# Kernel tuning notes

Measured on AMD Instinct MI355X. Metric: run time of the kernel, lower is better.

The kernel has to match this reference:

```python
import jax, jax.numpy as jnp
import numpy as np

D_MODEL, N_HEADS, N_KV, HEAD_DIM, D_LAT = 1024, 8, 2, 128, 32
N_REP = N_HEADS // N_KV  # 4
B, T = 2, 2048


def setup_inputs() -> dict:
    key = jax.random.key(0)
    ks = jax.random.split(key, 8)
    s = lambda fan_in: 1.0 / np.sqrt(fan_in)
    return {
        "x": jax.random.normal(ks[0], (B, T, D_MODEL), jnp.float32),
        # weights stored as [in, out] (transpose of torch Linear.weight)
        "wq": jax.random.normal(ks[1], (D_MODEL, N_HEADS * HEAD_DIM), jnp.float32) * s(D_MODEL),
        "wk_down": jax.random.normal(ks[2], (D_MODEL, N_KV * D_LAT), jnp.float32) * s(D_MODEL),
        "wv_down": jax.random.normal(ks[3], (D_MODEL, N_KV * D_LAT), jnp.float32) * s(D_MODEL),
        "wk_up": jax.random.normal(ks[4], (D_LAT, HEAD_DIM), jnp.float32) * s(D_LAT),
        "wv_up": jax.random.normal(ks[5], (D_LAT, HEAD_DIM), jnp.float32) * s(D_LAT),
        "wo": jax.random.normal(ks[6], (N_HEADS * HEAD_DIM, D_MODEL), jnp.float32) * s(N_HEADS * HEAD_DIM),
    }


def reference(x, wq, wk_down, wv_down, wk_up, wv_up, wo):
    Bq, Tq, _ = x.shape
    scale = HEAD_DIM ** -0.5  # SDPA default scale
    # Q: [B,T,Hkv,Rep,Dh] (grouped view avoids materializing repeated K/V)
    q = (x @ wq).reshape(Bq, Tq, N_KV, N_REP, HEAD_DIM)
    # latent KV: [B,T,Hkv,Dl] -> up-project to [B,T,Hkv,Dh]
    k_lat = (x @ wk_down).reshape(Bq, Tq, N_KV, D_LAT)
    v_lat = (x @ wv_down).reshape(Bq, Tq, N_KV, D_LAT)
    k = jnp.einsum("bkhl,ld->bkhd", k_lat, wk_up)
    v = jnp.einsum("bkhl,ld->bkhd", v_lat, wv_up)
    # causal attention, GQA via grouped einsum (no repeat_interleave copy)
    scores = jnp.einsum("bqhrd,bkhd->bhrqk", q, k) * scale  # [B,Hkv,Rep,T,T]
    causal = jnp.tril(jnp.ones((Tq, Tq), dtype=bool))
    scores = jnp.where(causal, scores, jnp.finfo(scores.dtype).min)
    probs = jax.nn.softmax(scores, axis=-1)
    y = jnp.einsum("bhrqk,bkhd->bqhrd", probs, v)  # [B,T,Hkv,Rep,Dh]
    y = y.reshape(Bq, Tq, N_HEADS * HEAD_DIM)
    return y @ wo
```

## Files before the change

### kernel.cpp

```cpp
#include <hip/hip_runtime.h>
#include <hip/hip_bf16.h>


typedef __bf16 bf16_t;
typedef bf16_t bf16x8 __attribute__((ext_vector_type(8)));
typedef float f32x4 __attribute__((ext_vector_type(4)));

__device__ inline bf16x8 cvt8(const float* __restrict__ p) {
  f32x4 a = *(const f32x4*)p, b = *(const f32x4*)(p + 4);
  bf16x8 r;
#pragma unroll
  for (int i = 0; i < 4; ++i) { r[i] = (bf16_t)a[i]; r[4 + i] = (bf16_t)b[i]; }
  return r;
}

__global__ __launch_bounds__(256) void prep_mfma(
    const float* __restrict__ x, const float* __restrict__ wq,
    const float* __restrict__ wkd, const float* __restrict__ wvd,
    const float* __restrict__ wku, const float* __restrict__ wvu,
    const float* __restrict__ wo, bf16_t* __restrict__ Xb,
    bf16_t* __restrict__ WqkvT, bf16_t* __restrict__ WcombT) {
  __shared__ __align__(16) char smem[34816];
  const int tid = threadIdx.x;
  const int wave = tid >> 6, lane = tid & 63;
  const int quad = lane >> 4, col = lane & 15;
  const int bi = blockIdx.x;

  if (bi < 64) {
    const int h = bi >> 3;
    const int c0 = (bi & 7) * 128 + wave * 32;
    f32x4 acc[2][2];
#pragma unroll
    for (int i = 0; i < 2; ++i)
#pragma unroll
      for (int j = 0; j < 2; ++j) acc[i][j] = (f32x4){0.f, 0.f, 0.f, 0.f};
#pragma unroll
    for (int ks = 0; ks < 4; ++ks) {
      const int ko = ks * 32 + quad * 8;
      bf16x8 a0 = cvt8(wku + col * 128 + ko);
      bf16x8 a1 = cvt8(wku + (16 + col) * 128 + ko);
      bf16x8 b0 = cvt8(wq + (size_t)(c0 + col) * 1024 + h * 128 + ko);
      bf16x8 b1 = cvt8(wq + (size_t)(c0 + 16 + col) * 1024 + h * 128 + ko);
      acc[0][0] = __builtin_amdgcn_mfma_f32_16x16x32_bf16(a0, b0, acc[0][0], 0, 0, 0);
      acc[0][1] = __builtin_amdgcn_mfma_f32_16x16x32_bf16(a0, b1, acc[0][1], 0, 0, 0);
      acc[1][0] = __builtin_amdgcn_mfma_f32_16x16x32_bf16(a1, b0, acc[1][0], 0, 0, 0);
      acc[1][1] = __builtin_amdgcn_mfma_f32_16x16x32_bf16(a1, b1, acc[1][1], 0, 0, 0);
    }
#pragma unroll
    for (int ms = 0; ms < 2; ++ms)
#pragma unroll
      for (int ns = 0; ns < 2; ++ns)
#pragma unroll
        for (int v = 0; v < 4; ++v)
          WqkvT[(size_t)(h * 32 + ms * 16 + quad * 4 + v) * 1024 + c0 + ns * 16 + col] =
              (bf16_t)acc[ms][ns][v];
  } else if (bi < 128) {
    const int b2 = bi - 64;
    const int h = b2 >> 3, m0 = (b2 & 7) * 128;
    bf16_t(*B_lds)[136] = (bf16_t(*)[136])smem;
    {
      const int d = tid >> 1, mh = (tid & 1) * 64;
      const float* wp = wo + (size_t)(h * 128 + d) * 1024 + m0 + mh;
#pragma unroll
      for (int i = 0; i < 16; ++i) {
        f32x4 w4 = *(const f32x4*)(wp + i * 4);
#pragma unroll
        for (int t = 0; t < 4; ++t) B_lds[mh + i * 4 + t][d] = (bf16_t)w4[t];
      }
    }
    __syncthreads();
    f32x4 acc[2][2];
#pragma unroll
    for (int i = 0; i < 2; ++i)
#pragma unroll
      for (int j = 0; j < 2; ++j) acc[i][j] = (f32x4){0.f, 0.f, 0.f, 0.f};
#pragma unroll
    for (int ks = 0; ks < 4; ++ks) {
      const int ko = ks * 32 + quad * 8;
      bf16x8 a0 = cvt8(wvu + col * 128 + ko);
      bf16x8 a1 = cvt8(wvu + (16 + col) * 128 + ko);
      bf16x8 b0 = *(const bf16x8*)&B_lds[wave * 32 + col][ko];
      bf16x8 b1 = *(const bf16x8*)&B_lds[wave * 32 + 16 + col][ko];
      acc[0][0] = __builtin_amdgcn_mfma_f32_16x16x32_bf16(a0, b0, acc[0][0], 0, 0, 0);
      acc[0][1] = __builtin_amdgcn_mfma_f32_16x16x32_bf16(a0, b1, acc[0][1], 0, 0, 0);
      acc[1][0] = __builtin_amdgcn_mfma_f32_16x16x32_bf16(a1, b0, acc[1][0], 0, 0, 0);
      acc[1][1] = __builtin_amdgcn_mfma_f32_16x16x32_bf16(a1, b1, acc[1][1], 0, 0, 0);
    }
#pragma unroll
    for (int ms = 0; ms < 2; ++ms)
#pragma unroll
      for (int ns = 0; ns < 2; ++ns)
#pragma unroll
        for (int v = 0; v < 4; ++v)
          WcombT[(size_t)(m0 + wave * 32 + ns * 16 + col) * 256 +
                 h * 32 + ms * 16 + quad * 4 + v] = (bf16_t)acc[ms][ns][v];
  } else if (bi < 160) {
    const int b3 = bi - 128;
    const int mat = b3 >> 4, c0 = (b3 & 15) * 64;
    const float* in = mat ? wvd : wkd;
    bf16_t(*tT)[72] = (bf16_t(*)[72])smem;
    {
      const int cc = tid >> 2, jq = (tid & 3) * 16;
      const float* ip = in + (size_t)(c0 + cc) * 64 + jq;
#pragma unroll
      for (int q = 0; q < 4; ++q) {
        f32x4 v4 = *(const f32x4*)(ip + q * 4);
#pragma unroll
        for (int t = 0; t < 4; ++t) tT[jq + q * 4 + t][cc] = (bf16_t)v4[t];
      }
    }
    __syncthreads();
    {
      const int j = tid >> 2, cq = (tid & 3) * 16;
      bf16_t* op = WqkvT + (size_t)(256 + mat * 64 + j) * 1024 + c0 + cq;
      *(bf16x8*)op = *(const bf16x8*)&tT[j][cq];
      *(bf16x8*)(op + 8) = *(const bf16x8*)&tT[j][cq + 8];
    }
  } else {
    const size_t base = (size_t)(bi - 160) * 32768;
    const float* ip = x + base;
    bf16_t* op = Xb + base;
#pragma unroll
    for (int it = 0; it < 16; ++it) {
      const int o = it * 2048 + tid * 8;
      *(bf16x8*)(op + o) = cvt8(ip + o);
    }
  }
}

__global__ __launch_bounds__(256) void gemm_qkv(
    const bf16_t* __restrict__ A, const bf16_t* __restrict__ Bt,
    bf16_t* __restrict__ C) {
  __shared__ bf16_t As[32][72];
  __shared__ bf16_t Bs[128][72];
  const int tid = threadIdx.x;
  const int wave = tid >> 6, lane = tid & 63;
  const int quad = lane >> 4, col = lane & 15;
  const int wm = (wave >> 1) * 16, wn = (wave & 1) * 64;
  const int m0 = blockIdx.y * 32, n0 = blockIdx.x * 128;

  f32x4 acc[4];
#pragma unroll
  for (int j = 0; j < 4; ++j) acc[j] = (f32x4){0.f, 0.f, 0.f, 0.f};

  const int ar = tid >> 3, ac = (tid & 7) * 8;
  const int br = tid >> 1, bc = (tid & 1) * 32;
  const bf16_t* aP = A + (size_t)(m0 + ar) * 1024 + ac;
  const bf16_t* bP = Bt + (size_t)(n0 + br) * 1024 + bc;

  bf16x8 aR0 = *(const bf16x8*)aP;
  bf16x8 bR0 = *(const bf16x8*)bP, bR1 = *(const bf16x8*)(bP + 8);
  bf16x8 bR2 = *(const bf16x8*)(bP + 16), bR3 = *(const bf16x8*)(bP + 24);

  for (int kt = 0; kt < 16; ++kt) {
    *(bf16x8*)&As[ar][ac] = aR0;
    *(bf16x8*)&Bs[br][bc] = bR0; *(bf16x8*)&Bs[br][bc + 8] = bR1;
    *(bf16x8*)&Bs[br][bc + 16] = bR2; *(bf16x8*)&Bs[br][bc + 24] = bR3;
    __syncthreads();
    if (kt < 15) {
      const int k0 = (kt + 1) * 64;
      aR0 = *(const bf16x8*)(aP + k0);
      bR0 = *(const bf16x8*)(bP + k0); bR1 = *(const bf16x8*)(bP + k0 + 8);
      bR2 = *(const bf16x8*)(bP + k0 + 16); bR3 = *(const bf16x8*)(bP + k0 + 24);
    }
#pragma unroll
    for (int ks = 0; ks < 2; ++ks) {
      bf16x8 af = *(const bf16x8*)&As[wm + col][ks * 32 + quad * 8];
      bf16x8 bfr[4];
#pragma unroll
      for (int j = 0; j < 4; ++j) bfr[j] = *(const bf16x8*)&Bs[wn + j * 16 + col][ks * 32 + quad * 8];
#pragma unroll
      for (int j = 0; j < 4; ++j)
        acc[j] = __builtin_amdgcn_mfma_f32_16x16x32_bf16(af, bfr[j], acc[j], 0, 0, 0);
    }
    __syncthreads();
  }

#pragma unroll
  for (int j = 0; j < 4; ++j) {
    const int cg = n0 + wn + j * 16 + col;
#pragma unroll
    for (int v = 0; v < 4; ++v)
      C[(size_t)(m0 + wm + quad * 4 + v) * 384 + cg] = (bf16_t)acc[j][v];
  }
}

__global__ __launch_bounds__(256) void gemm_out(
    const bf16_t* __restrict__ A, const bf16_t* __restrict__ Bt,
    float* __restrict__ C) {
  __shared__ bf16_t As[64][72];
  __shared__ bf16_t Bs[128][72];
  const int tid = threadIdx.x;
  const int wave = tid >> 6, lane = tid & 63;
  const int quad = lane >> 4, col = lane & 15;
  const int wm = (wave >> 1) * 32, wn = (wave & 1) * 64;
  const int m0 = blockIdx.y * 64, n0 = blockIdx.x * 128;

  f32x4 acc[2][4];
#pragma unroll
  for (int i = 0; i < 2; ++i)
#pragma unroll
    for (int j = 0; j < 4; ++j) acc[i][j] = (f32x4){0.f, 0.f, 0.f, 0.f};

  const int ar = tid >> 2, ac = (tid & 3) * 16;
  const int br = tid >> 1, bc = (tid & 1) * 32;
  const bf16_t* aP = A + (size_t)(m0 + ar) * 384 + ac;
  const bf16_t* bP = Bt + (size_t)(n0 + br) * 256 + bc;

  bf16x8 aR0 = *(const bf16x8*)aP, aR1 = *(const bf16x8*)(aP + 8);
  bf16x8 bR0 = *(const bf16x8*)bP, bR1 = *(const bf16x8*)(bP + 8);
  bf16x8 bR2 = *(const bf16x8*)(bP + 16), bR3 = *(const bf16x8*)(bP + 24);

  for (int kt = 0; kt < 4; ++kt) {
    *(bf16x8*)&As[ar][ac] = aR0; *(bf16x8*)&As[ar][ac + 8] = aR1;
    *(bf16x8*)&Bs[br][bc] = bR0; *(bf16x8*)&Bs[br][bc + 8] = bR1;
    *(bf16x8*)&Bs[br][bc + 16] = bR2; *(bf16x8*)&Bs[br][bc + 24] = bR3;
    __syncthreads();
    if (kt < 3) {
      const int k0 = (kt + 1) * 64;
      aR0 = *(const bf16x8*)(aP + k0); aR1 = *(const bf16x8*)(aP + k0 + 8);
      bR0 = *(const bf16x8*)(bP + k0); bR1 = *(const bf16x8*)(bP + k0 + 8);
      bR2 = *(const bf16x8*)(bP + k0 + 16); bR3 = *(const bf16x8*)(bP + k0 + 24);
    }
#pragma unroll
    for (int ks = 0; ks < 2; ++ks) {
      bf16x8 af[2], bfr[4];
#pragma unroll
      for (int i = 0; i < 2; ++i) af[i] = *(const bf16x8*)&As[wm + i * 16 + col][ks * 32 + quad * 8];
#pragma unroll
      for (int j = 0; j < 4; ++j) bfr[j] = *(const bf16x8*)&Bs[wn + j * 16 + col][ks * 32 + quad * 8];
#pragma unroll
      for (int i = 0; i < 2; ++i)
#pragma unroll
        for (int j = 0; j < 4; ++j)
          acc[i][j] = __builtin_amdgcn_mfma_f32_16x16x32_bf16(af[i], bfr[j], acc[i][j], 0, 0, 0);
    }
    __syncthreads();
  }

#pragma unroll
  for (int i = 0; i < 2; ++i) {
    const int rg = m0 + wm + i * 16 + quad * 4;
#pragma unroll
    for (int j = 0; j < 4; ++j) {
      const int cg = n0 + wn + j * 16 + col;
#pragma unroll
      for (int v = 0; v < 4; ++v)
        C[(size_t)(rg + v) * 1024 + cg] = acc[i][j][v];
    }
  }
}

__global__ __launch_bounds__(256, 3) void attn_lat(bf16_t* QKV) {
  const int bi = blockIdx.x;
  const int half = bi >> 8, rest = bi & 255;
  const int qt = half ? 127 - (rest >> 1) : (rest >> 1);
  const int hkv = rest & 1, b = half;
  const int tid = threadIdx.x;
  const int wave = tid >> 6, lane = tid & 63;
  const int quad = lane >> 4, col = lane & 15;

  __shared__ bf16_t Ks[2][128][36];
  __shared__ bf16_t Vt[2][32][132];
  __shared__ bf16_t Ps[4][16][132];

  const int qb = qt * 16;
  const size_t rowbase = (size_t)b * 2048;
  const int qcol0 = (hkv * 4 + wave) * 32;

  bf16x8 a_q = *(const bf16x8*)(QKV + (rowbase + qb + col) * 384 + qcol0 + quad * 8);

  f32x4 o0 = (f32x4){0.f, 0.f, 0.f, 0.f};
  f32x4 o1 = (f32x4){0.f, 0.f, 0.f, 0.f};
  float lsum[4] = {0.f, 0.f, 0.f, 0.f};

  const int nkt = (qb >> 7) + 1;
  const float scale = 0.08838834764831843f;

  const int kr = tid >> 1, dc = (tid & 1) * 16;
  const bf16_t* kvBase = QKV + (rowbase + kr) * 384 + 256 + hkv * 32 + dc;

  {
    bf16x8 kA = *(const bf16x8*)kvBase, kB = *(const bf16x8*)(kvBase + 8);
    bf16x8 vA = *(const bf16x8*)(kvBase + 64), vB = *(const bf16x8*)(kvBase + 72);
    *(bf16x8*)&Ks[0][kr][dc] = kA;
    *(bf16x8*)&Ks[0][kr][dc + 8] = kB;
#pragma unroll
    for (int t = 0; t < 8; ++t) { Vt[0][dc + t][kr] = vA[t]; Vt[0][dc + 8 + t][kr] = vB[t]; }
  }
  __syncthreads();

  for (int kt = 0; kt < nkt; ++kt) {
    const int cur = kt & 1;
    const int kb = kt * 128;
    const bool more = (kt + 1 < nkt);

    bf16x8 kA, kB, vA, vB;
    if (more) {
      const bf16_t* np = kvBase + (size_t)(kt + 1) * 128 * 384;
      kA = *(const bf16x8*)np; kB = *(const bf16x8*)(np + 8);
      vA = *(const bf16x8*)(np + 64); vB = *(const bf16x8*)(np + 72);
    }

    f32x4 s[8];
#pragma unroll
    for (int k8 = 0; k8 < 8; ++k8) {
      bf16x8 bk = *(const bf16x8*)&Ks[cur][k8 * 16 + col][quad * 8];
      s[k8] = __builtin_amdgcn_mfma_f32_16x16x32_bf16(a_q, bk, (f32x4){0.f, 0.f, 0.f, 0.f}, 0, 0, 0);
    }

    const bool full = (kb + 128 <= qb);
#pragma unroll
    for (int v = 0; v < 4; ++v) {
      const int qr = quad * 4 + v;
      const int qg = qb + qr;
#pragma unroll
      for (int k8 = 0; k8 < 8; ++k8) {
        float xx = s[k8][v] * scale;
        if (!full && (kb + k8 * 16 + col > qg)) xx = -1e30f;
        const float p = __expf(xx);
        lsum[v] += p;
        Ps[wave][qr][k8 * 16 + col] = (bf16_t)p;
      }
    }
    __asm__ __volatile__("" ::: "memory");

#pragma unroll
    for (int kc = 0; kc < 4; ++kc) {
      bf16x8 a_p = *(const bf16x8*)&Ps[wave][col][kc * 32 + quad * 8];
      bf16x8 bv0 = *(const bf16x8*)&Vt[cur][col][kc * 32 + quad * 8];
      bf16x8 bv1 = *(const bf16x8*)&Vt[cur][16 + col][kc * 32 + quad * 8];
      o0 = __builtin_amdgcn_mfma_f32_16x16x32_bf16(a_p, bv0, o0, 0, 0, 0);
      o1 = __builtin_amdgcn_mfma_f32_16x16x32_bf16(a_p, bv1, o1, 0, 0, 0);
    }

    if (more) {
      *(bf16x8*)&Ks[cur ^ 1][kr][dc] = kA;
      *(bf16x8*)&Ks[cur ^ 1][kr][dc + 8] = kB;
#pragma unroll
      for (int t = 0; t < 8; ++t) { Vt[cur ^ 1][dc + t][kr] = vA[t]; Vt[cur ^ 1][dc + 8 + t][kr] = vB[t]; }
    }
    __syncthreads();
  }

#pragma unroll
  for (int v = 0; v < 4; ++v) {
    float l = lsum[v];
#pragma unroll
    for (int off = 8; off; off >>= 1) l += __shfl_xor(l, off, 64);
    const float inv = 1.f / l;
    const size_t r = (rowbase + qb + quad * 4 + v) * 384 + qcol0;
    QKV[r + col] = (bf16_t)(o0[v] * inv);
    QKV[r + 16 + col] = (bf16_t)(o1[v] * inv);
  }
}

extern "C" void kernel_launch(void* const* d_in, const int* in_sizes, int n_in,
                              void* d_out, int out_size, void* d_ws, size_t ws_size,
                              hipStream_t stream) {
  (void)in_sizes; (void)n_in; (void)out_size; (void)ws_size;
  const float* x   = (const float*)d_in[0];
  const float* wq  = (const float*)d_in[1];
  const float* wkd = (const float*)d_in[2];
  const float* wvd = (const float*)d_in[3];
  const float* wku = (const float*)d_in[4];
  const float* wvu = (const float*)d_in[5];
  const float* wo  = (const float*)d_in[6];
  float* out = (float*)d_out;

  bf16_t* WqkvT  = (bf16_t*)d_ws;
  bf16_t* WcombT = WqkvT + (size_t)384 * 1024;
  bf16_t* QKV    = WcombT + (size_t)1024 * 256;
  bf16_t* Xb     = QKV + (size_t)4096 * 384;

  prep_mfma<<<288, 256, 0, stream>>>(x, wq, wkd, wvd, wku, wvu, wo, Xb, WqkvT, WcombT);
  gemm_qkv<<<dim3(3, 128), 256, 0, stream>>>(Xb, WqkvT, QKV);
  attn_lat<<<512, 256, 0, stream>>>(QKV);
  gemm_out<<<dim3(8, 64), 256, 0, stream>>>(QKV, WcombT, out);
}
```

Before: 137.3 us.

## Fuse four kernels into one cooperative persistent kernel with grid syncs

Merges the prep, QKV GEMM, latent attention and output GEMM kernels into a single cooperative kernel of 512 blocks. The stages are separated by grid.sync() and share one LDS union. The aim is to remove the launch gaps between kernels. In exchange, each stage is now limited to 512 resident blocks (two per CU), every block must wait at a grid-wide barrier, and the unbalanced causal attention stage still decides when the final GEMM can start.

Result: slower. 342.6 us (+149.5%).

```diff
diff --git a/kernel.cpp b/kernel.cpp
--- a/kernel.cpp
+++ b/kernel.cpp
@@ -1,6 +1,9 @@
 #include <hip/hip_runtime.h>
 #include <hip/hip_bf16.h>
-
+#include <hip/hip_cooperative_groups.h>
+
+
+namespace cg = cooperative_groups;
 
 typedef __bf16 bf16_t;
 typedef bf16_t bf16x8 __attribute__((ext_vector_type(8)));
@@ -14,13 +17,22 @@
   return r;
 }
 
-__global__ __launch_bounds__(256) void prep_mfma(
+__global__ __launch_bounds__(256, 2) void fused_mla(
     const float* __restrict__ x, const float* __restrict__ wq,
     const float* __restrict__ wkd, const float* __restrict__ wvd,
     const float* __restrict__ wku, const float* __restrict__ wvu,
     const float* __restrict__ wo, bf16_t* __restrict__ Xb,
-    bf16_t* __restrict__ WqkvT, bf16_t* __restrict__ WcombT) {
-  __shared__ __align__(16) char smem[34816];
+    bf16_t* __restrict__ WqkvT, bf16_t* __restrict__ WcombT,
+    bf16_t* __restrict__ QKV, float* __restrict__ out) {
+  cg::grid_group grid = cg::this_grid();
+
+  __shared__ __align__(16) union SM {
+    char prep[34816];
+    struct { bf16_t As[32][72]; bf16_t Bs[128][72]; } g1;
+    struct { bf16_t Ks[2][128][36]; bf16_t Vt[2][32][132]; bf16_t Ps[4][16][132]; } at;
+    struct { bf16_t As[64][72]; bf16_t Bs[128][72]; } g2;
+  } sm;
+
   const int tid = threadIdx.x;
   const int wave = tid >> 6, lane = tid & 63;
   const int quad = lane >> 4, col = lane & 15;
@@ -57,7 +69,7 @@
   } else if (bi < 128) {
     const int b2 = bi - 64;
     const int h = b2 >> 3, m0 = (b2 & 7) * 128;
-    bf16_t(*B_lds)[136] = (bf16_t(*)[136])smem;
+    bf16_t(*B_lds)[136] = (bf16_t(*)[136])sm.prep;
     {
       const int d = tid >> 1, mh = (tid & 1) * 64;
       const float* wp = wo + (size_t)(h * 128 + d) * 1024 + m0 + mh;
@@ -98,7 +110,7 @@
     const int b3 = bi - 128;
     const int mat = b3 >> 4, c0 = (b3 & 15) * 64;
     const float* in = mat ? wvd : wkd;
-    bf16_t(*tT)[72] = (bf16_t(*)[72])smem;
+    bf16_t(*tT)[72] = (bf16_t(*)[72])sm.prep;
     {
       const int cc = tid >> 2, jq = (tid & 3) * 16;
       const float* ip = in + (size_t)(c0 + cc) * 64 + jq;
@@ -117,241 +129,226 @@
       *(bf16x8*)(op + 8) = *(const bf16x8*)&tT[j][cq + 8];
     }
   } else {
-    const size_t base = (size_t)(bi - 160) * 32768;
-    const float* ip = x + base;
-    bf16_t* op = Xb + base;
-#pragma unroll
-    for (int it = 0; it < 16; ++it) {
-      const int o = it * 2048 + tid * 8;
-      *(bf16x8*)(op + o) = cvt8(ip + o);
+#pragma unroll
+    for (int it = 0; it < 6; ++it) {
+      const size_t off = ((size_t)(bi - 160) + (size_t)it * 352) * 2048 + (size_t)tid * 8;
+      if (off < (size_t)4096 * 1024) *(bf16x8*)(Xb + off) = cvt8(x + off);
     }
   }
-}
-
-__global__ __launch_bounds__(256) void gemm_qkv(
-    const bf16_t* __restrict__ A, const bf16_t* __restrict__ Bt,
-    bf16_t* __restrict__ C) {
-  __shared__ bf16_t As[32][72];
-  __shared__ bf16_t Bs[128][72];
-  const int tid = threadIdx.x;
-  const int wave = tid >> 6, lane = tid & 63;
-  const int quad = lane >> 4, col = lane & 15;
-  const int wm = (wave >> 1) * 16, wn = (wave & 1) * 64;
-  const int m0 = blockIdx.y * 32, n0 = blockIdx.x * 128;
-
-  f32x4 acc[4];
-#pragma unroll
-  for (int j = 0; j < 4; ++j) acc[j] = (f32x4){0.f, 0.f, 0.f, 0.f};
-
-  const int ar = tid >> 3, ac = (tid & 7) * 8;
-  const int br = tid >> 1, bc = (tid & 1) * 32;
-  const bf16_t* aP = A + (size_t)(m0 + ar) * 1024 + ac;
-  const bf16_t* bP = Bt + (size_t)(n0 + br) * 1024 + bc;
-
-  bf16x8 aR0 = *(const bf16x8*)aP;
-  bf16x8 bR0 = *(const bf16x8*)bP, bR1 = *(const bf16x8*)(bP + 8);
-  bf16x8 bR2 = *(const bf16x8*)(bP + 16), bR3 = *(const bf16x8*)(bP + 24);
-
-  for (int kt = 0; kt < 16; ++kt) {
-    *(bf16x8*)&As[ar][ac] = aR0;
-    *(bf16x8*)&Bs[br][bc] = bR0; *(bf16x8*)&Bs[br][bc + 8] = bR1;
-    *(bf16x8*)&Bs[br][bc + 16] = bR2; *(bf16x8*)&Bs[br][bc + 24] = bR3;
+  grid.sync();
+
+  if (bi < 384) {
+    auto& As = sm.g1.As;
+    auto& Bs = sm.g1.Bs;
+    const int wm = (wave >> 1) * 16, wn = (wave & 1) * 64;
+    const int n0 = (bi % 3) * 128, m0 = (bi / 3) * 32;
+
+    f32x4 acc[4];
+#pragma unroll
+    for (int j = 0; j < 4; ++j) acc[j] = (f32x4){0.f, 0.f, 0.f, 0.f};
+
+    const int ar = tid >> 3, ac = (tid & 7) * 8;
+    const int br = tid >> 1, bc = (tid & 1) * 32;
+    const bf16_t* aP = Xb + (size_t)(m0 + ar) * 1024 + ac;
+    const bf16_t* bP = WqkvT + (size_t)(n0 + br) * 1024 + bc;
+
+    bf16x8 aR0 = *(const bf16x8*)aP;
+    bf16x8 bR0 = *(const bf16x8*)bP, bR1 = *(const bf16x8*)(bP + 8);
+    bf16x8 bR2 = *(const bf16x8*)(bP + 16), bR3 = *(const bf16x8*)(bP + 24);
+
+    for (int kt = 0; kt < 16; ++kt) {
+      *(bf16x8*)&As[ar][ac] = aR0;
+      *(bf16x8*)&Bs[br][bc] = bR0; *(bf16x8*)&Bs[br][bc + 8] = bR1;
+      *(bf16x8*)&Bs[br][bc + 16] = bR2; *(bf16x8*)&Bs[br][bc + 24] = bR3;
+      __syncthreads();
+      if (kt < 15) {
+        const int k0 = (kt + 1) * 64;
+        aR0 = *(const bf16x8*)(aP + k0);
+        bR0 = *(const bf16x8*)(bP + k0); bR1 = *(const bf16x8*)(bP + k0 + 8);
+        bR2 = *(const bf16x8*)(bP + k0 + 16); bR3 = *(const bf16x8*)(bP + k0 + 24);
+      }
+#pragma unroll
+      for (int ks = 0; ks < 2; ++ks) {
+        bf16x8 af = *(const bf16x8*)&As[wm + col][ks * 32 + quad * 8];
+        bf16x8 bfr[4];
+#pragma unroll
+        for (int j = 0; j < 4; ++j) bfr[j] = *(const bf16x8*)&Bs[wn + j * 16 + col][ks * 32 + quad * 8];
+#pragma unroll
+        for (int j = 0; j < 4; ++j)
+          acc[j] = __builtin_amdgcn_mfma_f32_16x16x32_bf16(af, bfr[j], acc[j], 0, 0, 0);
+      }
+      __syncthreads();
+    }
+
+#pragma unroll
+    for (int j = 0; j < 4; ++j) {
+      const int cg_ = n0 + wn + j * 16 + col;
+#pragma unroll
+      for (int v = 0; v < 4; ++v)
+        QKV[(size_t)(m0 + wm + quad * 4 + v) * 384 + cg_] = (bf16_t)acc[j][v];
+    }
+  }
+  grid.sync();
+
+  {
+    auto& Ks = sm.at.Ks;
+    auto& Vt = sm.at.Vt;
+    auto& Ps = sm.at.Ps;
+    const int half = bi >> 8, rest = bi & 255;
+    const int qt = half ? 127 - (rest >> 1) : (rest >> 1);
+    const int hkv = rest & 1, b = half;
+
+    const int qb = qt * 16;
+    const size_t rowbase = (size_t)b * 2048;
+    const int qcol0 = (hkv * 4 + wave) * 32;
+
+    bf16x8 a_q = *(const bf16x8*)(QKV + (rowbase + qb + col) * 384 + qcol0 + quad * 8);
+
+    f32x4 o0 = (f32x4){0.f, 0.f, 0.f, 0.f};
+    f32x4 o1 = (f32x4){0.f, 0.f, 0.f, 0.f};
+    float lsum[4] = {0.f, 0.f, 0.f, 0.f};
+
+    const int nkt = (qb >> 7) + 1;
+    const float scale = 0.08838834764831843f;
+
+    const int kr = tid >> 1, dc = (tid & 1) * 16;
+    const bf16_t* kvBase = QKV + (rowbase + kr) * 384 + 256 + hkv * 32 + dc;
+
+    {
+      bf16x8 kA = *(const bf16x8*)kvBase, kB = *(const bf16x8*)(kvBase + 8);
+      bf16x8 vA = *(const bf16x8*)(kvBase + 64), vB = *(const bf16x8*)(kvBase + 72);
+      *(bf16x8*)&Ks[0][kr][dc] = kA;
+      *(bf16x8*)&Ks[0][kr][dc + 8] = kB;
+#pragma unroll
+      for (int t = 0; t < 8; ++t) { Vt[0][dc + t][kr] = vA[t]; Vt[0][dc + 8 + t][kr] = vB[t]; }
+    }
     __syncthreads();
-    if (kt < 15) {
-      const int k0 = (kt + 1) * 64;
-      aR0 = *(const bf16x8*)(aP + k0);
-      bR0 = *(const bf16x8*)(bP + k0); bR1 = *(const bf16x8*)(bP + k0 + 8);
-      bR2 = *(const bf16x8*)(bP + k0 + 16); bR3 = *(const bf16x8*)(bP + k0 + 24);
-    }
-#pragma unroll
-    for (int ks = 0; ks < 2; ++ks) {
-      bf16x8 af = *(const bf16x8*)&As[wm + col][ks * 32 + quad * 8];
-      bf16x8 bfr[4];
-#pragma unroll
-      for (int j = 0; j < 4; ++j) bfr[j] = *(const bf16x8*)&Bs[wn + j * 16 + col][ks * 32 + quad * 8];
-#pragma unroll
-      for (int j = 0; j < 4; ++j)
-        acc[j] = __builtin_amdgcn_mfma_f32_16x16x32_bf16(af, bfr[j], acc[j], 0, 0, 0);
-    }
-    __syncthreads();
+
+    for (int kt = 0; kt < nkt; ++kt) {
+      const int cur = kt & 1;
+      const int kb = kt * 128;
+      const bool more = (kt + 1 < nkt);
+
+      bf16x8 kA, kB, vA, vB;
+      if (more) {
+        const bf16_t* np = kvBase + (size_t)(kt + 1) * 128 * 384;
+        kA = *(const bf16x8*)np; kB = *(const bf16x8*)(np + 8);
+        vA = *(const bf16x8*)(np + 64); vB = *(const bf16x8*)(np + 72);
+      }
+
+      f32x4 s[8];
+#pragma unroll
+      for (int k8 = 0; k8 < 8; ++k8) {
+        bf16x8 bk = *(const bf16x8*)&Ks[cur][k8 * 16 + col][quad * 8];
+        s[k8] = __builtin_amdgcn_mfma_f32_16x16x32_bf16(a_q, bk, (f32x4){0.f, 0.f, 0.f, 0.f}, 0, 0, 0);
+      }
+
+      const bool full = (kb + 128 <= qb);
+#pragma unroll
+      for (int v = 0; v < 4; ++v) {
+        const int qr = quad * 4 + v;
+        const int qg = qb + qr;
+#pragma unroll
+        for (int k8 = 0; k8 < 8; ++k8) {
+          float xx = s[k8][v] * scale;
+          if (!full && (kb + k8 * 16 + col > qg)) xx = -1e30f;
+          const float p = __expf(xx);
+          lsum[v] += p;
+          Ps[wave][qr][k8 * 16 + col] = (bf16_t)p;
+        }
+      }
+      __asm__ __volatile__("" ::: "memory");
+
+#pragma unroll
+      for (int kc = 0; kc < 4; ++kc) {
+        bf16x8 a_p = *(const bf16x8*)&Ps[wave][col][kc * 32 + quad * 8];
+        bf16x8 bv0 = *(const bf16x8*)&Vt[cur][col][kc * 32 + quad * 8];
+        bf16x8 bv1 = *(const bf16x8*)&Vt[cur][16 + col][kc * 32 + quad * 8];
+        o0 = __builtin_amdgcn_mfma_f32_16x16x32_bf16(a_p, bv0, o0, 0, 0, 0);
+        o1 = __builtin_amdgcn_mfma_f32_16x16x32_bf16(a_p, bv1, o1, 0, 0, 0);
+      }
+
+      if (more) {
+        *(bf16x8*)&Ks[cur ^ 1][kr][dc] = kA;
+        *(bf16x8*)&Ks[cur ^ 1][kr][dc + 8] = kB;
+#pragma unroll
+        for (int t = 0; t < 8; ++t) { Vt[cur ^ 1][dc + t][kr] = vA[t]; Vt[cur ^ 1][dc + 8 + t][kr] = vB[t]; }
+      }
+      __syncthreads();
+    }
+
+#pragma unroll
+    for (int v = 0; v < 4; ++v) {
+      float l = lsum[v];
+#pragma unroll
+      for (int off = 8; off; off >>= 1) l += __shfl_xor(l, off, 64);
+      const float inv = 1.f / l;
+      const size_t r = (rowbase + qb + quad * 4 + v) * 384 + qcol0;
+      QKV[r + col] = (bf16_t)(o0[v] * inv);
+      QKV[r + 16 + col] = (bf16_t)(o1[v] * inv);
+    }
   }
-
-#pragma unroll
-  for (int j = 0; j < 4; ++j) {
-    const int cg = n0 + wn + j * 16 + col;
-#pragma unroll
-    for (int v = 0; v < 4; ++v)
-      C[(size_t)(m0 + wm + quad * 4 + v) * 384 + cg] = (bf16_t)acc[j][v];
-  }
-}
-
-__global__ __launch_bounds__(256) void gemm_out(
-    const bf16_t* __restrict__ A, const bf16_t* __restrict__ Bt,
-    float* __restrict__ C) {
-  __shared__ bf16_t As[64][72];
-  __shared__ bf16_t Bs[128][72];
-  const int tid = threadIdx.x;
-  const int wave = tid >> 6, lane = tid & 63;
-  const int quad = lane >> 4, col = lane & 15;
-  const int wm = (wave >> 1) * 32, wn = (wave & 1) * 64;
-  const int m0 = blockIdx.y * 64, n0 = blockIdx.x * 128;
-
-  f32x4 acc[2][4];
-#pragma unroll
-  for (int i = 0; i < 2; ++i)
-#pragma unroll
-    for (int j = 0; j < 4; ++j) acc[i][j] = (f32x4){0.f, 0.f, 0.f, 0.f};
-
-  const int ar = tid >> 2, ac = (tid & 3) * 16;
-  const int br = tid >> 1, bc = (tid & 1) * 32;
-  const bf16_t* aP = A + (size_t)(m0 + ar) * 384 + ac;
-  const bf16_t* bP = Bt + (size_t)(n0 + br) * 256 + bc;
-
-  bf16x8 aR0 = *(const bf16x8*)aP, aR1 = *(const bf16x8*)(aP + 8);
-  bf16x8 bR0 = *(const bf16x8*)bP, bR1 = *(const bf16x8*)(bP + 8);
-  bf16x8 bR2 = *(const bf16x8*)(bP + 16), bR3 = *(const bf16x8*)(bP + 24);
-
-  for (int kt = 0; kt < 4; ++kt) {
-    *(bf16x8*)&As[ar][ac] = aR0; *(bf16x8*)&As[ar][ac + 8] = aR1;
-    *(bf16x8*)&Bs[br][bc] = bR0; *(bf16x8*)&Bs[br][bc + 8] = bR1;
-    *(bf16x8*)&Bs[br][bc + 16] = bR2; *(bf16x8*)&Bs[br][bc + 24] = bR3;
-    __syncthreads();
-    if (kt < 3) {
-      const int k0 = (kt + 1) * 64;
-      aR0 = *(const bf16x8*)(aP + k0); aR1 = *(const bf16x8*)(aP + k0 + 8);
-      bR0 = *(const bf16x8*)(bP + k0); bR1 = *(const bf16x8*)(bP + k0 + 8);
-      bR2 = *(const bf16x8*)(bP + k0 + 16); bR3 = *(const bf16x8*)(bP + k0 + 24);
-    }
-#pragma unroll
-    for (int ks = 0; ks < 2; ++ks) {
-      bf16x8 af[2], bfr[4];
-#pragma unroll
-      for (int i = 0; i < 2; ++i) af[i] = *(const bf16x8*)&As[wm + i * 16 + col][ks * 32 + quad * 8];
-#pragma unroll
-      for (int j = 0; j < 4; ++j) bfr[j] = *(const bf16x8*)&Bs[wn + j * 16 + col][ks * 32 + quad * 8];
-#pragma unroll
-      for (int i = 0; i < 2; ++i)
-#pragma unroll
-        for (int j = 0; j < 4; ++j)
-          acc[i][j] = __builtin_amdgcn_mfma_f32_16x16x32_bf16(af[i], bfr[j], acc[i][j], 0, 0, 0);
-    }
-    __syncthreads();
-  }
-
-#pragma unroll
-  for (int i = 0; i < 2; ++i) {
-    const int rg = m0 + wm + i * 16 + quad * 4;
-#pragma unroll
-    for (int j = 0; j < 4; ++j) {
-      const int cg = n0 + wn + j * 16 + col;
-#pragma unroll
-      for (int v = 0; v < 4; ++v)
-        C[(size_t)(rg + v) * 1024 + cg] = acc[i][j][v];
-    }
-  }
-}
-
-__global__ __launch_bounds__(256, 3) void attn_lat(bf16_t* QKV) {
-  const int bi = blockIdx.x;
-  const int half = bi >> 8, rest = bi & 255;
-  const int qt = half ? 127 - (rest >> 1) : (rest >> 1);
-  const int hkv = rest & 1, b = half;
-  const int tid = threadIdx.x;
-  const int wave = tid >> 6, lane = tid & 63;
-  const int quad = lane >> 4, col = lane & 15;
-
-  __shared__ bf16_t Ks[2][128][36];
-  __shared__ bf16_t Vt[2][32][132];
-  __shared__ bf16_t Ps[4][16][132];
-
-  const int qb = qt * 16;
-  const size_t rowbase = (size_t)b * 2048;
-  const int qcol0 = (hkv * 4 + wave) * 32;
-
-  bf16x8 a_q = *(const bf16x8*)(QKV + (rowbase + qb + col) * 384 + qcol0 + quad * 8);
-
-  f32x4 o0 = (f32x4){0.f, 0.f, 0.f, 0.f};
-  f32x4 o1 = (f32x4){0.f, 0.f, 0.f, 0.f};
-  float lsum[4] = {0.f, 0.f, 0.f, 0.f};
-
-  const int nkt = (qb >> 7) + 1;
-  const float scale = 0.08838834764831843f;
-
-  const int kr = tid >> 1, dc = (tid & 1) * 16;
-  const bf16_t* kvBase = QKV + (rowbase + kr) * 384 + 256 + hkv * 32 + dc;
+  grid.sync();
 
   {
-    bf16x8 kA = *(const bf16x8*)kvBase, kB = *(const bf16x8*)(kvBase + 8);
-    bf16x8 vA = *(const bf16x8*)(kvBase + 64), vB = *(const bf16x8*)(kvBase + 72);
-    *(bf16x8*)&Ks[0][kr][dc] = kA;
-    *(bf16x8*)&Ks[0][kr][dc + 8] = kB;
-#pragma unroll
-    for (int t = 0; t < 8; ++t) { Vt[0][dc + t][kr] = vA[t]; Vt[0][dc + 8 + t][kr] = vB[t]; }
-  }
-  __syncthreads();
-
-  for (int kt = 0; kt < nkt; ++kt) {
-    const int cur = kt & 1;
-    const int kb = kt * 128;
-    const bool more = (kt + 1 < nkt);
-
-    bf16x8 kA, kB, vA, vB;
-    if (more) {
-      const bf16_t* np = kvBase + (size_t)(kt + 1) * 128 * 384;
-      kA = *(const bf16x8*)np; kB = *(const bf16x8*)(np + 8);
-      vA = *(const bf16x8*)(np + 64); vB = *(const bf16x8*)(np + 72);
-    }
-
-    f32x4 s[8];
-#pragma unroll
-    for (int k8 = 0; k8 < 8; ++k8) {
-      bf16x8 bk = *(const bf16x8*)&Ks[cur][k8 * 16 + col][quad * 8];
-      s[k8] = __builtin_amdgcn_mfma_f32_16x16x32_bf16(a_q, bk, (f32x4){0.f, 0.f, 0.f, 0.f}, 0, 0, 0);
-    }
-
-    const bool full = (kb + 128 <= qb);
-#pragma unroll
-    for (int v = 0; v < 4; ++v) {
-      const int qr = quad * 4 + v;
-      const int qg = qb + qr;
-#pragma unroll
-      for (int k8 = 0; k8 < 8; ++k8) {
-        float xx = s[k8][v] * scale;
-        if (!full && (kb + k8 * 16 + col > qg)) xx = -1e30f;
-        const float p = __expf(xx);
-        lsum[v] += p;
-        Ps[wave][qr][k8 * 16 + col] = (bf16_t)p;
-      }
-    }
-    __asm__ __volatile__("" ::: "memory");
-
-#pragma unroll
-    for (int kc = 0; kc < 4; ++kc) {
-      bf16x8 a_p = *(const bf16x8*)&Ps[wave][col][kc * 32 + quad * 8];
-      bf16x8 bv0 = *(const bf16x8*)&Vt[cur][col][kc * 32 + quad * 8];
-      bf16x8 bv1 = *(const bf16x8*)&Vt[cur][16 + col][kc * 32 + quad * 8];
-      o0 = __builtin_amdgcn_mfma_f32_16x16x32_bf16(a_p, bv0, o0, 0, 0, 0);
-      o1 = __builtin_amdgcn_mfma_f32_16x16x32_bf16(a_p, bv1, o1, 0, 0, 0);
-    }
-
-    if (more) {
-      *(bf16x8*)&Ks[cur ^ 1][kr][dc] = kA;
-      *(bf16x8*)&Ks[cur ^ 1][kr][dc + 8] = kB;
-#pragma unroll
-      for (int t = 0; t < 8; ++t) { Vt[cur ^ 1][dc + t][kr] = vA[t]; Vt[cur ^ 1][dc + 8 + t][kr] = vB[t]; }
-    }
-    __syncthreads();
-  }
-
-#pragma unroll
-  for (int v = 0; v < 4; ++v) {
-    float l = lsum[v];
-#pragma unroll
-    for (int off = 8; off; off >>= 1) l += __shfl_xor(l, off, 64);
-    const float inv = 1.f / l;
-    const size_t r = (rowbase + qb + quad * 4 + v) * 384 + qcol0;
-    QKV[r + col] = (bf16_t)(o0[v] * inv);
-    QKV[r + 16 + col] = (bf16_t)(o1[v] * inv);
+    auto& As = sm.g2.As;
+    auto& Bs = sm.g2.Bs;
+    const int wm = (wave >> 1) * 32, wn = (wave & 1) * 64;
+    const int m0 = (bi >> 3) * 64, n0 = (bi & 7) * 128;
+
+    f32x4 acc[2][4];
+#pragma unroll
+    for (int i = 0; i < 2; ++i)
+#pragma unroll
+      for (int j = 0; j < 4; ++j) acc[i][j] = (f32x4){0.f, 0.f, 0.f, 0.f};
+
+    const int ar = tid >> 2, ac = (tid & 3) * 16;
+    const int br = tid >> 1, bc = (tid & 1) * 32;
+    const bf16_t* aP = QKV + (size_t)(m0 + ar) * 384 + ac;
+    const bf16_t* bP = WcombT + (size_t)(n0 + br) * 256 + bc;
+
+    bf16x8 aR0 = *(const bf16x8*)aP, aR1 = *(const bf16x8*)(aP + 8);
+    bf16x8 bR0 = *(const bf16x8*)bP, bR1 = *(const bf16x8*)(bP + 8);
+    bf16x8 bR2 = *(const bf16x8*)(bP + 16), bR3 = *(const bf16x8*)(bP + 24);
+
+    for (int kt = 0; kt < 4; ++kt) {
+      *(bf16x8*)&As[ar][ac] = aR0; *(bf16x8*)&As[ar][ac + 8] = aR1;
+      *(bf16x8*)&Bs[br][bc] = bR0; *(bf16x8*)&Bs[br][bc + 8] = bR1;
+      *(bf16x8*)&Bs[br][bc + 16] = bR2; *(bf16x8*)&Bs[br][bc + 24] = bR3;
+      __syncthreads();
+      if (kt < 3) {
+        const int k0 = (kt + 1) * 64;
+        aR0 = *(const bf16x8*)(aP + k0); aR1 = *(const bf16x8*)(aP + k0 + 8);
+        bR0 = *(const bf16x8*)(bP + k0); bR1 = *(const bf16x8*)(bP + k0 + 8);
+        bR2 = *(const bf16x8*)(bP + k0 + 16); bR3 = *(const bf16x8*)(bP + k0 + 24);
+      }
+#pragma unroll
+      for (int ks = 0; ks < 2; ++ks) {
+        bf16x8 af[2], bfr[4];
+#pragma unroll
+        for (int i = 0; i < 2; ++i) af[i] = *(const bf16x8*)&As[wm + i * 16 + col][ks * 32 + quad * 8];
+#pragma unroll
+        for (int j = 0; j < 4; ++j) bfr[j] = *(const bf16x8*)&Bs[wn + j * 16 + col][ks * 32 + quad * 8];
+#pragma unroll
+        for (int i = 0; i < 2; ++i)
+#pragma unroll
+          for (int j = 0; j < 4; ++j)
+            acc[i][j] = __builtin_amdgcn_mfma_f32_16x16x32_bf16(af[i], bfr[j], acc[i][j], 0, 0, 0);
+      }
+      __syncthreads();
+    }
+
+#pragma unroll
+    for (int i = 0; i < 2; ++i) {
+      const int rg = m0 + wm + i * 16 + quad * 4;
+#pragma unroll
+      for (int j = 0; j < 4; ++j) {
+        const int cg_ = n0 + wn + j * 16 + col;
+#pragma unroll
+        for (int v = 0; v < 4; ++v)
+          out[(size_t)(rg + v) * 1024 + cg_] = acc[i][j][v];
+      }
+    }
   }
 }
 
@@ -373,8 +370,9 @@
   bf16_t* QKV    = WcombT + (size_t)1024 * 256;
   bf16_t* Xb     = QKV + (size_t)4096 * 384;
 
-  prep_mfma<<<288, 256, 0, stream>>>(x, wq, wkd, wvd, wku, wvu, wo, Xb, WqkvT, WcombT);
-  gemm_qkv<<<dim3(3, 128), 256, 0, stream>>>(Xb, WqkvT, QKV);
-  attn_lat<<<512, 256, 0, stream>>>(QKV);
-  gemm_out<<<dim3(8, 64), 256, 0, stream>>>(QKV, WcombT, out);
+  void* args[] = {(void*)&x, (void*)&wq, (void*)&wkd, (void*)&wvd,
+                  (void*)&wku, (void*)&wvu, (void*)&wo, (void*)&Xb,
+                  (void*)&WqkvT, (void*)&WcombT, (void*)&QKV, (void*)&out};
+  hipLaunchCooperativeKernel((const void*)fused_mla, dim3(512), dim3(256),
+                             args, 0, stream);
 }
```
